# Optimization experiments

Measured on AMD Instinct MI355X. Metric: run time of the kernel, lower is better.

## Reference

```python
import jax, jax.numpy as jnp
import numpy as np

EPS = 1e-5
QMAX = 127.0


def setup_inputs() -> dict:
    key = jax.random.key(0)
    k1, k2, k3, k4, k5 = jax.random.split(key, 5)
    B, S, N = 2, 4096, 4096
    x1 = jax.random.normal(k1, (B, S, N), dtype=jnp.float32)
    x2 = jax.random.normal(k2, (B, S, N), dtype=jnp.float32)
    gamma = jax.random.normal(k3, (N,), dtype=jnp.float32)
    # smoothing scales are positive channel-wise multipliers
    smooth_scale1 = jax.random.uniform(k4, (N,), dtype=jnp.float32, minval=0.5, maxval=1.5)
    smooth_scale2 = jax.random.uniform(k5, (N,), dtype=jnp.float32, minval=0.5, maxval=1.5)
    return {"x1": x1, "x2": x2, "gamma": gamma,
            "smooth_scale1": smooth_scale1, "smooth_scale2": smooth_scale2}


def _dynamic_quant(y, smooth_scale):
    # per-row (last-axis) dynamic symmetric int8 quantization after smoothing
    ys = y * smooth_scale                       # [..., N]
    scale = jnp.max(jnp.abs(ys), axis=-1, keepdims=True) / QMAX  # [..., 1]
    yq = jnp.clip(jnp.round(ys / scale), -128.0, 127.0).astype(jnp.int8)
    return yq, scale[..., 0]


def reference(x1, x2, gamma, smooth_scale1, smooth_scale2):
    # fused residual add
    x_sum = x1 + x2                             # [B, S, N]
    # RMSNorm over the last axis with weight gamma
    inv_rms = jax.lax.rsqrt(jnp.mean(x_sum * x_sum, axis=-1, keepdims=True) + EPS)
    y_norm = x_sum * inv_rms * gamma            # [B, S, N]
    # dual smooth-quant with independent dynamic per-row scales
    y1, scale1 = _dynamic_quant(y_norm, smooth_scale1)
    y2, scale2 = _dynamic_quant(y_norm, smooth_scale2)
    return (x_sum, y_norm, y1, scale1, y2, scale2)
```

## Files before the change

### kernel.cpp

```cpp
#include <hip/hip_runtime.h>

#define NCOLS 4096
#define QMAXF 127.0f
#define EPSF 1e-5f

typedef float f4 __attribute__((ext_vector_type(4)));

__global__ __launch_bounds__(256) void fused_addrms_dualquant(
    const float* __restrict__ x1,
    const float* __restrict__ x2,
    const float* __restrict__ gamma,
    const float* __restrict__ sm1,
    const float* __restrict__ sm2,
    float* __restrict__ o_xsum,
    float* __restrict__ o_ynorm,
    float* __restrict__ o_y1,
    float* __restrict__ o_s1,
    float* __restrict__ o_y2,
    float* __restrict__ o_s2)
{
    const int row = blockIdx.x;
    const long long base = (long long)row * NCOLS;
    const int t = threadIdx.x;

    f4 v[4];
    float ssq = 0.f, a1 = 0.f, a2 = 0.f;

#pragma unroll
    for (int c = 0; c < 4; ++c) {
        const int idx = c * 1024 + t * 4;
        f4 xa = __builtin_nontemporal_load((const f4*)(x1 + base + idx));
        f4 xb = __builtin_nontemporal_load((const f4*)(x2 + base + idx));
        f4 s = xa + xb;
        v[c] = s;
        ssq += s.x * s.x + s.y * s.y + s.z * s.z + s.w * s.w;
        __builtin_nontemporal_store(s, (f4*)(o_xsum + base + idx));

        f4 g  = *(const f4*)(gamma + idx);
        f4 m1 = *(const f4*)(sm1 + idx);
        f4 m2 = *(const f4*)(sm2 + idx);
        f4 gg = s * g;
        f4 p1 = gg * m1;
        f4 p2 = gg * m2;
        a1 = fmaxf(a1, fmaxf(fmaxf(fabsf(p1.x), fabsf(p1.y)),
                             fmaxf(fabsf(p1.z), fabsf(p1.w))));
        a2 = fmaxf(a2, fmaxf(fmaxf(fabsf(p2.x), fabsf(p2.y)),
                             fmaxf(fabsf(p2.z), fabsf(p2.w))));
    }

#pragma unroll
    for (int off = 32; off > 0; off >>= 1) {
        ssq += __shfl_down(ssq, off);
        a1 = fmaxf(a1, __shfl_down(a1, off));
        a2 = fmaxf(a2, __shfl_down(a2, off));
    }

    __shared__ float red[12];
    __shared__ float bc[3];
    if ((t & 63) == 0) {
        const int w = t >> 6;
        red[w]     = ssq;
        red[4 + w] = a1;
        red[8 + w] = a2;
    }
    __syncthreads();
    if (t == 0) {
        float tot = red[0] + red[1] + red[2] + red[3];
        float invrms = rsqrtf(tot * (1.0f / (float)NCOLS) + EPSF);
        float am1 = fmaxf(fmaxf(red[4], red[5]), fmaxf(red[6], red[7])) * invrms;
        float am2 = fmaxf(fmaxf(red[8], red[9]), fmaxf(red[10], red[11])) * invrms;
        float sc1 = am1 / QMAXF;
        float sc2 = am2 / QMAXF;
        o_s1[row] = sc1;
        o_s2[row] = sc2;
        bc[0] = invrms;
        bc[1] = 1.0f / sc1;
        bc[2] = 1.0f / sc2;
    }
    __syncthreads();
    const float invrms = bc[0];
    const float r1 = bc[1];
    const float r2 = bc[2];

#pragma unroll
    for (int c = 0; c < 4; ++c) {
        const int idx = c * 1024 + t * 4;
        f4 g  = *(const f4*)(gamma + idx);
        f4 m1 = *(const f4*)(sm1 + idx);
        f4 m2 = *(const f4*)(sm2 + idx);

        f4 y = v[c] * invrms * g;
        __builtin_nontemporal_store(y, (f4*)(o_ynorm + base + idx));

        f4 ys1 = y * m1;
        f4 ys2 = y * m2;
        f4 q1, q2;
        q1.x = fminf(fmaxf(rintf(ys1.x * r1), -128.f), 127.f);
        q1.y = fminf(fmaxf(rintf(ys1.y * r1), -128.f), 127.f);
        q1.z = fminf(fmaxf(rintf(ys1.z * r1), -128.f), 127.f);
        q1.w = fminf(fmaxf(rintf(ys1.w * r1), -128.f), 127.f);
        q2.x = fminf(fmaxf(rintf(ys2.x * r2), -128.f), 127.f);
        q2.y = fminf(fmaxf(rintf(ys2.y * r2), -128.f), 127.f);
        q2.z = fminf(fmaxf(rintf(ys2.z * r2), -128.f), 127.f);
        q2.w = fminf(fmaxf(rintf(ys2.w * r2), -128.f), 127.f);
        __builtin_nontemporal_store(q1, (f4*)(o_y1 + base + idx));
        __builtin_nontemporal_store(q2, (f4*)(o_y2 + base + idx));
    }
}

extern "C" void kernel_launch(void* const* d_in, const int* in_sizes, int n_in,
                              void* d_out, int out_size, void* d_ws, size_t ws_size,
                              hipStream_t stream) {
    const float* x1    = (const float*)d_in[0];
    const float* x2    = (const float*)d_in[1];
    const float* gamma = (const float*)d_in[2];
    const float* sm1   = (const float*)d_in[3];
    const float* sm2   = (const float*)d_in[4];

    const long long n_elem = in_sizes[0];
    const int ncols = in_sizes[2];
    const long long rows = n_elem / ncols;

    float* out = (float*)d_out;
    float* o_xsum  = out;
    float* o_ynorm = out + n_elem;
    float* o_y1    = out + 2 * n_elem;
    float* o_s1    = out + 3 * n_elem;
    float* o_y2    = o_s1 + rows;
    float* o_s2    = o_y2 + n_elem;

    fused_addrms_dualquant<<<dim3((unsigned)rows), dim3(256), 0, stream>>>(
        x1, x2, gamma, sm1, sm2, o_xsum, o_ynorm, o_y1, o_s1, o_y2, o_s2);
}
```

Before: 687.1 us.

## Split fused kernel into per-row stats pass and grid-stride quantize pass

Replaces the single row-per-block kernel with two kernels when a workspace is available. The first uses one wavefront per row to compute the residual sum, RMS and quant scales, writing xsum with ordinary (cached) stores and per-row stats to the workspace. The second is a grid-stride elementwise kernel that re-reads xsum, then writes ynorm and both quantized outputs. The split removes block-level syncs and register-held row data, but adds a full extra read of xsum (about 128 MB) and a second launch. The bet is that this traffic is served partly from cache.

Result: no change. 695.9 us (+1.3%).

```diff
diff --git a/kernel.cpp b/kernel.cpp
--- a/kernel.cpp
+++ b/kernel.cpp
@@ -6,36 +6,28 @@
 
 typedef float f4 __attribute__((ext_vector_type(4)));
 
-__global__ __launch_bounds__(256) void fused_addrms_dualquant(
-    const float* __restrict__ x1,
-    const float* __restrict__ x2,
-    const float* __restrict__ gamma,
-    const float* __restrict__ sm1,
+__global__ __launch_bounds__(256) void phaseA_stats(
+    const float* __restrict__ x1, const float* __restrict__ x2,
+    const float* __restrict__ gamma, const float* __restrict__ sm1,
     const float* __restrict__ sm2,
-    float* __restrict__ o_xsum,
-    float* __restrict__ o_ynorm,
-    float* __restrict__ o_y1,
-    float* __restrict__ o_s1,
-    float* __restrict__ o_y2,
-    float* __restrict__ o_s2)
+    float* __restrict__ o_xsum, float* __restrict__ o_s1, float* __restrict__ o_s2,
+    float* __restrict__ ws_inv, float* __restrict__ ws_r1, float* __restrict__ ws_r2,
+    int rows)
 {
-    const int row = blockIdx.x;
-    const long long base = (long long)row * NCOLS;
-    const int t = threadIdx.x;
-
-    f4 v[4];
+    const int wid  = (int)((blockIdx.x * 256u + threadIdx.x) >> 6);
+    if (wid >= rows) return;
+    const int lane = threadIdx.x & 63;
+    const long long base = (long long)wid * NCOLS;
+
     float ssq = 0.f, a1 = 0.f, a2 = 0.f;
-
-#pragma unroll
-    for (int c = 0; c < 4; ++c) {
-        const int idx = c * 1024 + t * 4;
+#pragma unroll
+    for (int c = 0; c < 16; ++c) {
+        const int idx = c * 256 + lane * 4;
         f4 xa = __builtin_nontemporal_load((const f4*)(x1 + base + idx));
         f4 xb = __builtin_nontemporal_load((const f4*)(x2 + base + idx));
         f4 s = xa + xb;
-        v[c] = s;
+        *(f4*)(o_xsum + base + idx) = s;
         ssq += s.x * s.x + s.y * s.y + s.z * s.z + s.w * s.w;
-        __builtin_nontemporal_store(s, (f4*)(o_xsum + base + idx));
-
         f4 g  = *(const f4*)(gamma + idx);
         f4 m1 = *(const f4*)(sm1 + idx);
         f4 m2 = *(const f4*)(sm2 + idx);
@@ -55,13 +47,104 @@
         a2 = fmaxf(a2, __shfl_down(a2, off));
     }
 
+    if (lane == 0) {
+        float invrms = rsqrtf(ssq * (1.0f / (float)NCOLS) + EPSF);
+        float am1 = a1 * invrms;
+        float am2 = a2 * invrms;
+        float sc1 = am1 / QMAXF;
+        float sc2 = am2 / QMAXF;
+        o_s1[wid] = sc1;
+        o_s2[wid] = sc2;
+        ws_inv[wid] = invrms;
+        ws_r1[wid] = 1.0f / sc1;
+        ws_r2[wid] = 1.0f / sc2;
+    }
+}
+
+__global__ __launch_bounds__(256) void phaseB_quant(
+    const float* __restrict__ xsum, const float* __restrict__ gamma,
+    const float* __restrict__ sm1, const float* __restrict__ sm2,
+    const float* __restrict__ ws_inv, const float* __restrict__ ws_r1,
+    const float* __restrict__ ws_r2,
+    float* __restrict__ o_ynorm, float* __restrict__ o_y1, float* __restrict__ o_y2,
+    long long n4)
+{
+    const long long stride = (long long)gridDim.x * 256;
+    for (long long i = (long long)blockIdx.x * 256 + threadIdx.x; i < n4; i += stride) {
+        const int row  = (int)(i >> 10);
+        const int col4 = (int)(i & 1023);
+        f4 v = ((const f4*)xsum)[i];
+        const float invrms = ws_inv[row];
+        const float r1 = ws_r1[row];
+        const float r2 = ws_r2[row];
+        f4 g  = ((const f4*)gamma)[col4];
+        f4 m1 = ((const f4*)sm1)[col4];
+        f4 m2 = ((const f4*)sm2)[col4];
+
+        f4 y = v * invrms * g;
+        __builtin_nontemporal_store(y, (f4*)o_ynorm + i);
+
+        f4 ys1 = y * m1;
+        f4 ys2 = y * m2;
+        f4 q1, q2;
+        q1.x = fminf(fmaxf(rintf(ys1.x * r1), -128.f), 127.f);
+        q1.y = fminf(fmaxf(rintf(ys1.y * r1), -128.f), 127.f);
+        q1.z = fminf(fmaxf(rintf(ys1.z * r1), -128.f), 127.f);
+        q1.w = fminf(fmaxf(rintf(ys1.w * r1), -128.f), 127.f);
+        q2.x = fminf(fmaxf(rintf(ys2.x * r2), -128.f), 127.f);
+        q2.y = fminf(fmaxf(rintf(ys2.y * r2), -128.f), 127.f);
+        q2.z = fminf(fmaxf(rintf(ys2.z * r2), -128.f), 127.f);
+        q2.w = fminf(fmaxf(rintf(ys2.w * r2), -128.f), 127.f);
+        __builtin_nontemporal_store(q1, (f4*)o_y1 + i);
+        __builtin_nontemporal_store(q2, (f4*)o_y2 + i);
+    }
+}
+
+__global__ __launch_bounds__(256) void fused_addrms_dualquant(
+    const float* __restrict__ x1, const float* __restrict__ x2,
+    const float* __restrict__ gamma, const float* __restrict__ sm1,
+    const float* __restrict__ sm2,
+    float* __restrict__ o_xsum, float* __restrict__ o_ynorm,
+    float* __restrict__ o_y1, float* __restrict__ o_s1,
+    float* __restrict__ o_y2, float* __restrict__ o_s2)
+{
+    const int row = blockIdx.x;
+    const long long base = (long long)row * NCOLS;
+    const int t = threadIdx.x;
+
+    f4 v[4];
+    float ssq = 0.f, a1 = 0.f, a2 = 0.f;
+#pragma unroll
+    for (int c = 0; c < 4; ++c) {
+        const int idx = c * 1024 + t * 4;
+        f4 xa = __builtin_nontemporal_load((const f4*)(x1 + base + idx));
+        f4 xb = __builtin_nontemporal_load((const f4*)(x2 + base + idx));
+        f4 s = xa + xb;
+        v[c] = s;
+        ssq += s.x * s.x + s.y * s.y + s.z * s.z + s.w * s.w;
+        __builtin_nontemporal_store(s, (f4*)(o_xsum + base + idx));
+        f4 g  = *(const f4*)(gamma + idx);
+        f4 m1 = *(const f4*)(sm1 + idx);
+        f4 m2 = *(const f4*)(sm2 + idx);
+        f4 gg = s * g;
+        f4 p1 = gg * m1;
+        f4 p2 = gg * m2;
+        a1 = fmaxf(a1, fmaxf(fmaxf(fabsf(p1.x), fabsf(p1.y)),
+                             fmaxf(fabsf(p1.z), fabsf(p1.w))));
+        a2 = fmaxf(a2, fmaxf(fmaxf(fabsf(p2.x), fabsf(p2.y)),
+                             fmaxf(fabsf(p2.z), fabsf(p2.w))));
+    }
+#pragma unroll
+    for (int off = 32; off > 0; off >>= 1) {
+        ssq += __shfl_down(ssq, off);
+        a1 = fmaxf(a1, __shfl_down(a1, off));
+        a2 = fmaxf(a2, __shfl_down(a2, off));
+    }
     __shared__ float red[12];
     __shared__ float bc[3];
     if ((t & 63) == 0) {
         const int w = t >> 6;
-        red[w]     = ssq;
-        red[4 + w] = a1;
-        red[8 + w] = a2;
+        red[w] = ssq; red[4 + w] = a1; red[8 + w] = a2;
     }
     __syncthreads();
     if (t == 0) {
@@ -71,27 +154,21 @@
         float am2 = fmaxf(fmaxf(red[8], red[9]), fmaxf(red[10], red[11])) * invrms;
         float sc1 = am1 / QMAXF;
         float sc2 = am2 / QMAXF;
-        o_s1[row] = sc1;
-        o_s2[row] = sc2;
-        bc[0] = invrms;
-        bc[1] = 1.0f / sc1;
-        bc[2] = 1.0f / sc2;
+        o_s1[row] = sc1; o_s2[row] = sc2;
+        bc[0] = invrms; bc[1] = 1.0f / sc1; bc[2] = 1.0f / sc2;
     }
     __syncthreads();
     const float invrms = bc[0];
     const float r1 = bc[1];
     const float r2 = bc[2];
-
 #pragma unroll
     for (int c = 0; c < 4; ++c) {
         const int idx = c * 1024 + t * 4;
         f4 g  = *(const f4*)(gamma + idx);
         f4 m1 = *(const f4*)(sm1 + idx);
         f4 m2 = *(const f4*)(sm2 + idx);
-
         f4 y = v[c] * invrms * g;
         __builtin_nontemporal_store(y, (f4*)(o_ynorm + base + idx));
-
         f4 ys1 = y * m1;
         f4 ys2 = y * m2;
         f4 q1, q2;
@@ -129,6 +206,22 @@
     float* o_y2    = o_s1 + rows;
     float* o_s2    = o_y2 + n_elem;
 
-    fused_addrms_dualquant<<<dim3((unsigned)rows), dim3(256), 0, stream>>>(
-        x1, x2, gamma, sm1, sm2, o_xsum, o_ynorm, o_y1, o_s1, o_y2, o_s2);
-}
+    const size_t need = (size_t)(3 * rows) * sizeof(float);
+    if (d_ws != nullptr && ws_size >= need) {
+        float* wsf = (float*)d_ws;
+        float* ws_inv = wsf;
+        float* ws_r1  = wsf + rows;
+        float* ws_r2  = wsf + 2 * rows;
+        const int blocksA = (int)((rows + 3) / 4);
+        phaseA_stats<<<dim3(blocksA), dim3(256), 0, stream>>>(
+            x1, x2, gamma, sm1, sm2, o_xsum, o_s1, o_s2,
+            ws_inv, ws_r1, ws_r2, (int)rows);
+        const long long n4 = n_elem / 4;
+        phaseB_quant<<<dim3(2048), dim3(256), 0, stream>>>(
+            o_xsum, gamma, sm1, sm2, ws_inv, ws_r1, ws_r2,
+            o_ynorm, o_y1, o_y2, n4);
+    } else {
+        fused_addrms_dualquant<<<dim3((unsigned)rows), dim3(256), 0, stream>>>(
+            x1, x2, gamma, sm1, sm2, o_xsum, o_ynorm, o_y1, o_s1, o_y2, o_s2);
+    }
+}
```
